# Optimization experiments

Hardware: AMD Instinct MI355X
Metric: run time of the kernel (lower is better)

Reference implementation:

```python
import jax, jax.numpy as jnp
import numpy as np

N_HEAD = 12
D_HEAD = 64
ROT_DIM = 32
THETA = 10000.0
LOOK_B = 1
LOOK_F = 1


def _rope(t):
    # t: [b, h, n, d]; interleaved RoPE on first ROT_DIM dims (lucidrains convention)
    n = t.shape[-2]
    inv_freq = 1.0 / (THETA ** (jnp.arange(0, ROT_DIM, 2, dtype=jnp.float32) / ROT_DIM))
    freqs = jnp.arange(n, dtype=jnp.float32)[:, None] * inv_freq[None, :]   # [n, ROT_DIM//2]
    freqs = jnp.repeat(freqs, 2, axis=-1)                                   # [n, ROT_DIM]
    cos, sin = jnp.cos(freqs), jnp.sin(freqs)
    t_rot, t_pass = t[..., :ROT_DIM], t[..., ROT_DIM:]
    pair = t_rot.reshape(*t_rot.shape[:-1], ROT_DIM // 2, 2)
    rot = jnp.stack([-pair[..., 1], pair[..., 0]], axis=-1).reshape(t_rot.shape)
    return jnp.concatenate([t_rot * cos + rot * sin, t_pass], axis=-1)


def _look_around(x, backward=LOOK_B, forward=LOOK_F, pad_value=-1, dim=2):
    # x: [B, w, n, ...]; pad the window axis, gather shifted windows, concat along dim
    w = x.shape[1]
    pad_width = [(0, 0)] * x.ndim
    pad_width[1] = (backward, forward)
    padded = jnp.pad(x, pad_width, constant_values=pad_value)
    return jnp.concatenate([padded[:, i:i + w] for i in range(forward + backward + 1)], axis=dim)


def _forward(x, w_attn, b_attn, window_size):
    b, n, d_model = x.shape
    qkv = x @ w_attn + b_attn                       # [b, n, 3*d_model]
    q, k, v = jnp.split(qkv, 3, axis=-1)

    def split_heads(t):
        return t.reshape(b, n, N_HEAD, D_HEAD).transpose(0, 2, 1, 3)  # [b, h, n, dh]

    q, k, v = split_heads(q), split_heads(k), split_heads(v)
    q, k = _rope(q), _rope(k)

    scale = D_HEAD ** -0.5
    B = b * N_HEAD
    w = n // window_size
    bq = q.reshape(B, w, window_size, D_HEAD) * scale
    bk = _look_around(k.reshape(B, w, window_size, D_HEAD), pad_value=-1.0)
    bv = _look_around(v.reshape(B, w, window_size, D_HEAD), pad_value=-1.0)

    seq = jnp.arange(n).reshape(1, w, window_size)
    bq_k = _look_around(seq, pad_value=-1)          # [1, w, (lb+lf+1)*ws]
    pad_mask = (bq_k == -1)[:, :, None, :]          # [1, w, 1, j]

    sim = jnp.einsum('bwie,bwje->bwij', bq, bk)     # [B, w, ws, (lb+lf+1)*ws]
    sim = jnp.where(pad_mask, -jnp.finfo(sim.dtype).max, sim)
    attn = jax.nn.softmax(sim, axis=-1)
    out = jnp.einsum('bwij,bwje->bwie', attn, bv)   # [B, w, ws, dh]
    out = out.reshape(b, N_HEAD, n, D_HEAD).transpose(0, 2, 1, 3).reshape(b, n, N_HEAD * D_HEAD)
    return out


def setup_inputs() -> dict:
    key = jax.random.key(0)
    k1, k2, k3 = jax.random.split(key, 3)
    d_model = 768
    x = jax.random.normal(k1, (4, 4096, d_model), dtype=jnp.float32)
    w_attn = jax.random.normal(k2, (d_model, 3 * d_model), dtype=jnp.float32) * 0.02
    b_attn = jax.random.normal(k3, (3 * d_model,), dtype=jnp.float32) * 0.02
    return {"x": x, "w_attn": w_attn, "b_attn": b_attn, "window_size": 128}


def reference(x, w_attn, b_attn, window_size):
    return _forward(x, w_attn, b_attn, window_size)
```

## Files before the change

kernel.cpp:

```cpp
#include <hip/hip_runtime.h>

typedef __attribute__((ext_vector_type(8))) short short8;
typedef __attribute__((ext_vector_type(16))) float f32x16;
typedef __attribute__((ext_vector_type(4))) float f32x4;

__device__ __forceinline__ unsigned short f2bf(float f) {
  unsigned int u = __float_as_uint(f);
  u += 0x7FFFu + ((u >> 16) & 1u);
  return (unsigned short)(u >> 16);
}
__device__ __forceinline__ float bf2f(unsigned short u) {
  return __uint_as_float(((unsigned int)u) << 16);
}

__device__ __forceinline__ void gload16(const unsigned short* g, unsigned short* l) {
  __builtin_amdgcn_global_load_lds(
      (const __attribute__((address_space(1))) void*)g,
      (__attribute__((address_space(3))) void*)l, 16, 0, 0);
}

__global__ __launch_bounds__(256) void cast_x_kernel(const float* __restrict__ x,
                                                     unsigned short* __restrict__ xb,
                                                     int n4) {
  int i = blockIdx.x * 256 + threadIdx.x;
  if (i >= n4) return;
  float4 v = ((const float4*)x)[i];
  ushort4 o;
  o.x = f2bf(v.x); o.y = f2bf(v.y); o.z = f2bf(v.z); o.w = f2bf(v.w);
  ((ushort4*)xb)[i] = o;
}

__global__ void transpose_w_kernel(const float* __restrict__ w,
                                   unsigned short* __restrict__ wt) {
  __shared__ float tile[32][33];
  int n0 = blockIdx.x * 32;
  int k0 = blockIdx.y * 32;
  for (int i = threadIdx.y; i < 32; i += 8)
    tile[i][threadIdx.x] = w[(size_t)(k0 + i) * 2304 + n0 + threadIdx.x];
  __syncthreads();
  for (int i = threadIdx.y; i < 32; i += 8)
    wt[(size_t)(n0 + i) * 768 + k0 + threadIdx.x] = f2bf(tile[threadIdx.x][i]);
}

__global__ __launch_bounds__(256) void qkv_gemm_kernel(
    const unsigned short* __restrict__ xb,
    const unsigned short* __restrict__ wt,
    const float* __restrict__ bias,
    unsigned short* __restrict__ Qb,
    unsigned short* __restrict__ Kb,
    unsigned short* __restrict__ Vb) {
  __shared__ unsigned short lA[128 * 64];
  __shared__ unsigned short lB[128 * 64];
  int bid = blockIdx.x;
  int swz = (bid & 7) * 288 + (bid >> 3);
  int mt = swz / 18, nt = swz - mt * 18;
  int m0 = mt * 128, n0 = nt * 128;

  int tid = threadIdx.x;
  int lane = tid & 63, wid = tid >> 6;
  int wr = wid >> 1, wc = wid & 1;
  int lr = lane & 15, lg = lane >> 4;
  int lswz = lr & 7;

  int offA[4], offB[4];
  unsigned short* ldsA[4];
  unsigned short* ldsB[4];
#pragma unroll
  for (int i = 0; i < 4; i++) {
    int gi = (wid * 4 + i) * 64 + lane;
    int r = gi >> 3;
    int gcl = (gi & 7) ^ (r & 7);
    offA[i] = (m0 + r) * 768 + gcl * 8;
    offB[i] = (n0 + r) * 768 + gcl * 8;
    ldsA[i] = &lA[(wid * 4 + i) * 512];
    ldsB[i] = &lB[(wid * 4 + i) * 512];
  }

  f32x4 acc[4][4] = {};
  const int rowA = (wr * 64 + lr) * 64;
  const int rowB = (wc * 64 + lr) * 64;

  for (int k0 = 0; k0 < 768; k0 += 64) {
    __syncthreads();
#pragma unroll
    for (int i = 0; i < 4; i++) gload16(xb + offA[i] + k0, ldsA[i]);
#pragma unroll
    for (int i = 0; i < 4; i++) gload16(wt + offB[i] + k0, ldsB[i]);
    __syncthreads();

    short8 af[4][2], bfr[4][2];
#pragma unroll
    for (int ks = 0; ks < 2; ks++) {
      int c = ((ks * 4 + lg) ^ lswz) * 8;
#pragma unroll
      for (int mi = 0; mi < 4; mi++)
        af[mi][ks] = *(const short8*)(&lA[rowA + mi * 1024 + c]);
#pragma unroll
      for (int ni = 0; ni < 4; ni++)
        bfr[ni][ks] = *(const short8*)(&lB[rowB + ni * 1024 + c]);
    }
#pragma unroll
    for (int ks = 0; ks < 2; ks++)
#pragma unroll
      for (int mi = 0; mi < 4; mi++)
#pragma unroll
        for (int ni = 0; ni < 4; ni++)
          acc[mi][ni] = __builtin_amdgcn_mfma_f32_16x16x32_bf16(af[mi][ks], bfr[ni][ks], acc[mi][ni], 0, 0, 0);
  }

#pragma unroll
  for (int ni = 0; ni < 4; ni++) {
    int n = n0 + wc * 64 + ni * 16 + lr;
    float bv = bias[n];
    int which = n / 768;
    int idx = n - which * 768;
    int h = idx >> 6, d = idx & 63;
    float scl = (which == 0) ? 0.125f : 1.0f;
    bool doRope = (which < 2) && (ni < 2);
    bool isHi = (d & 1);
    const float L2T = 13.287712379549449f;
    float invf = exp2f(-(float)((d >> 1) & 15) * (L2T / 16.0f));
    unsigned short* dst = (which == 0) ? Qb : ((which == 1) ? Kb : Vb);
#pragma unroll
    for (int mi = 0; mi < 4; mi++) {
#pragma unroll
      for (int reg = 0; reg < 4; reg++) {
        int m = m0 + wr * 64 + mi * 16 + lg * 4 + reg;
        int b = m >> 12, t = m & 4095;
        float val = acc[mi][ni][reg] + bv;
        if (doRope) {
          float other = __shfl_xor(val, 1, 64);
          float ang = (float)t * invf;
          float s, c;
          __sincosf(ang, &s, &c);
          val = isHi ? (val * c + other * s) : (val * c - other * s);
        }
        dst[(((size_t)(b * 12 + h)) * 4096 + t) * 64 + d] = f2bf(val * scl);
      }
    }
  }
}

#define KV_S 72
__global__ __launch_bounds__(256) void attn_kernel(
    const unsigned short* __restrict__ Qb,
    const unsigned short* __restrict__ Kb,
    const unsigned short* __restrict__ Vb,
    float* __restrict__ out) {
  __shared__ unsigned short kS[64 * KV_S];
  __shared__ unsigned short vS[64 * KV_S];
  int wi = blockIdx.x;
  int bh = blockIdx.y;
  int b = bh / 12, h = bh - b * 12;
  int tid = threadIdx.x, lane = tid & 63, wid = tid >> 6;
  int l31 = lane & 31, hi = lane >> 5;

  int qb0 = wi * 128 + wid * 32;
  const unsigned short* Qrow = Qb + ((size_t)bh * 4096 + qb0) * 64;
  short8 qf[4];
#pragma unroll
  for (int kk = 0; kk < 4; kk++)
    qf[kk] = *(const short8*)(Qrow + (size_t)l31 * 64 + kk * 16 + hi * 8);

  f32x16 oacc[2];
#pragma unroll
  for (int dt = 0; dt < 2; dt++)
#pragma unroll
    for (int r = 0; r < 16; r++) oacc[dt][r] = 0.0f;
  float mrow = -1e30f, lsum = 0.0f;

  const unsigned short* Kbase = Kb + (size_t)bh * 4096 * 64;
  const unsigned short* Vbase = Vb + (size_t)bh * 4096 * 64;

  int vk = tid & 63;
  int vq = tid >> 6;

  for (int c = 0; c < 6; c++) {
    int kp0 = (wi - 1) * 128 + c * 64;
    if (kp0 < 0 || kp0 >= 4096) continue;

    __syncthreads();
#pragma unroll
    for (int ci = tid; ci < 512; ci += 256) {
      int kk = ci >> 3, co = (ci & 7) * 8;
      *(uint4*)(&kS[kk * KV_S + co]) = *(const uint4*)(Kbase + (size_t)(kp0 + kk) * 64 + co);
    }
    {
      const unsigned short* vp = Vbase + (size_t)(kp0 + vk) * 64 + vq * 16;
      uint4 v0 = *(const uint4*)(vp);
      uint4 v1 = *(const uint4*)(vp + 8);
      const unsigned short* e = (const unsigned short*)&v0;
#pragma unroll
      for (int i = 0; i < 8; i++) vS[(vq * 16 + i) * KV_S + vk] = e[i];
      e = (const unsigned short*)&v1;
#pragma unroll
      for (int i = 0; i < 8; i++) vS[(vq * 16 + 8 + i) * KV_S + vk] = e[i];
    }
    __syncthreads();

    f32x16 s[2];
#pragma unroll
    for (int kt = 0; kt < 2; kt++) {
      f32x16 acc;
#pragma unroll
      for (int r = 0; r < 16; r++) acc[r] = 0.0f;
#pragma unroll
      for (int kk = 0; kk < 4; kk++) {
        short8 kf = *(const short8*)(&kS[(kt * 32 + l31) * KV_S + kk * 16 + hi * 8]);
        acc = __builtin_amdgcn_mfma_f32_32x32x16_bf16(kf, qf[kk], acc, 0, 0, 0);
      }
      s[kt] = acc;
    }

    float vmax = -1e30f;
#pragma unroll
    for (int kt = 0; kt < 2; kt++)
#pragma unroll
      for (int r = 0; r < 16; r++) vmax = fmaxf(vmax, s[kt][r]);
    vmax = fmaxf(vmax, __shfl_xor(vmax, 32, 64));
    float mnew = fmaxf(mrow, vmax);
    float corr = __expf(mrow - mnew);
    mrow = mnew;
    float rs = 0.0f;
#pragma unroll
    for (int kt = 0; kt < 2; kt++)
#pragma unroll
      for (int r = 0; r < 16; r++) {
        float p = __expf(s[kt][r] - mnew);
        s[kt][r] = p;
        rs += p;
      }
    rs += __shfl_xor(rs, 32, 64);
    lsum = lsum * corr + rs;
#pragma unroll
    for (int dt = 0; dt < 2; dt++)
#pragma unroll
      for (int r = 0; r < 16; r++) oacc[dt][r] *= corr;

#pragma unroll
    for (int kt = 0; kt < 2; kt++) {
#pragma unroll
      for (int kk = 0; kk < 2; kk++) {
        unsigned a0, a1, b0, b1;
        asm("v_cvt_pk_bf16_f32 %0, %1, %2" : "=v"(a0) : "v"(s[kt][kk * 8 + 0]), "v"(s[kt][kk * 8 + 1]));
        asm("v_cvt_pk_bf16_f32 %0, %1, %2" : "=v"(a1) : "v"(s[kt][kk * 8 + 2]), "v"(s[kt][kk * 8 + 3]));
        asm("v_cvt_pk_bf16_f32 %0, %1, %2" : "=v"(b0) : "v"(s[kt][kk * 8 + 4]), "v"(s[kt][kk * 8 + 5]));
        asm("v_cvt_pk_bf16_f32 %0, %1, %2" : "=v"(b1) : "v"(s[kt][kk * 8 + 6]), "v"(s[kt][kk * 8 + 7]));
        asm("v_permlane32_swap_b32 %0, %1" : "+v"(a0), "+v"(b0));
        asm("v_permlane32_swap_b32 %0, %1" : "+v"(a1), "+v"(b1));
        union { unsigned u[4]; short8 v; } pb;
        pb.u[0] = a0; pb.u[1] = a1; pb.u[2] = b0; pb.u[3] = b1;
#pragma unroll
        for (int dt = 0; dt < 2; dt++) {
          short8 vf = *(const short8*)(&vS[(dt * 32 + l31) * KV_S + kt * 32 + kk * 16 + hi * 8]);
          oacc[dt] = __builtin_amdgcn_mfma_f32_32x32x16_bf16(vf, pb.v, oacc[dt], 0, 0, 0);
        }
      }
    }
  }

  float inv = 1.0f / lsum;
  float* orow = out + ((size_t)b * 4096 + qb0 + l31) * 768 + h * 64;
#pragma unroll
  for (int dt = 0; dt < 2; dt++)
#pragma unroll
    for (int g = 0; g < 4; g++) {
      float4 o;
      o.x = oacc[dt][g * 4 + 0] * inv;
      o.y = oacc[dt][g * 4 + 1] * inv;
      o.z = oacc[dt][g * 4 + 2] * inv;
      o.w = oacc[dt][g * 4 + 3] * inv;
      *(float4*)(orow + dt * 32 + g * 8 + hi * 4) = o;
    }
}

extern "C" void kernel_launch(void* const* d_in, const int* in_sizes, int n_in,
                              void* d_out, int out_size, void* d_ws, size_t ws_size,
                              hipStream_t stream) {
  const float* x = (const float*)d_in[0];
  const float* w = (const float*)d_in[1];
  const float* bias = (const float*)d_in[2];
  float* out = (float*)d_out;

  char* ws = (char*)d_ws;
  unsigned short* xb = (unsigned short*)ws;
  unsigned short* wt = (unsigned short*)(ws + 25165824);
  unsigned short* Qb = (unsigned short*)(ws + 28704768);
  unsigned short* Kb = Qb + 12582912;
  unsigned short* Vb = Kb + 12582912;

  hipLaunchKernelGGL(cast_x_kernel, dim3(12288), dim3(256), 0, stream, x, xb, 3145728);
  hipLaunchKernelGGL(transpose_w_kernel, dim3(72, 24), dim3(32, 8), 0, stream, w, wt);
  hipLaunchKernelGGL(qkv_gemm_kernel, dim3(2304), dim3(256), 0, stream, xb, wt, bias, Qb, Kb, Vb);
  hipLaunchKernelGGL(attn_kernel, dim3(32, 48), dim3(256), 0, stream, Qb, Kb, Vb, out);
}
```

Baseline: 144.6 us.

## Restructure QKV GEMM into 256x256 tiles with triple-buffered async LDS pipeline

The QKV projection GEMM now uses 256x256 output tiles with 512 threads (8 waves, each computing 128x64), and a K-step of 32. A three-stage LDS ring buffer is filled by global_load_lds prefetches two steps ahead, using vmcnt waits and raw barriers in place of full __syncthreads. Loads for the next stage are interleaved between the two halves of the MFMA work, and s_setprio is raised around the MFMA blocks. This aims to hide global-memory latency and cut barrier stalls and redundant operand loads. In exchange it uses more registers per thread (32 accumulator fragments) and launches fewer blocks, which can limit occupancy.

```diff
diff --git a/kernel.cpp b/kernel.cpp
--- a/kernel.cpp
+++ b/kernel.cpp
@@ -17,6 +17,12 @@
   __builtin_amdgcn_global_load_lds(
       (const __attribute__((address_space(1))) void*)g,
       (__attribute__((address_space(3))) void*)l, 16, 0, 0);
+}
+
+__device__ __forceinline__ void barrier_raw() {
+  asm volatile("" ::: "memory");
+  __builtin_amdgcn_s_barrier();
+  asm volatile("" ::: "memory");
 }
 
 __global__ __launch_bounds__(256) void cast_x_kernel(const float* __restrict__ x,
@@ -42,100 +48,125 @@
     wt[(size_t)(n0 + i) * 768 + k0 + threadIdx.x] = f2bf(tile[threadIdx.x][i]);
 }
 
-__global__ __launch_bounds__(256) void qkv_gemm_kernel(
+__global__ __launch_bounds__(512, 2) void qkv_gemm_kernel(
     const unsigned short* __restrict__ xb,
     const unsigned short* __restrict__ wt,
     const float* __restrict__ bias,
     unsigned short* __restrict__ Qb,
     unsigned short* __restrict__ Kb,
     unsigned short* __restrict__ Vb) {
-  __shared__ unsigned short lA[128 * 64];
-  __shared__ unsigned short lB[128 * 64];
+  __shared__ unsigned short sA[3][256 * 32];
+  __shared__ unsigned short sB[3][256 * 32];
   int bid = blockIdx.x;
-  int swz = (bid & 7) * 288 + (bid >> 3);
-  int mt = swz / 18, nt = swz - mt * 18;
-  int m0 = mt * 128, n0 = nt * 128;
-
-  int tid = threadIdx.x;
-  int lane = tid & 63, wid = tid >> 6;
-  int wr = wid >> 1, wc = wid & 1;
+  int swz = (bid & 7) * 72 + (bid >> 3);
+  int mt = swz / 9, nt = swz - mt * 9;
+  int m0 = mt * 256, n0 = nt * 256;
+
+  int tid = threadIdx.x, lane = tid & 63, wid = tid >> 6;
+  int wr = wid >> 2, wcn = wid & 3;
   int lr = lane & 15, lg = lane >> 4;
-  int lswz = lr & 7;
-
-  int offA[4], offB[4];
-  unsigned short* ldsA[4];
-  unsigned short* ldsB[4];
-#pragma unroll
-  for (int i = 0; i < 4; i++) {
-    int gi = (wid * 4 + i) * 64 + lane;
-    int r = gi >> 3;
-    int gcl = (gi & 7) ^ (r & 7);
-    offA[i] = (m0 + r) * 768 + gcl * 8;
-    offB[i] = (n0 + r) * 768 + gcl * 8;
-    ldsA[i] = &lA[(wid * 4 + i) * 512];
-    ldsB[i] = &lB[(wid * 4 + i) * 512];
+
+  int srcA[2], srcB[2], dstO[2];
+#pragma unroll
+  for (int j = 0; j < 2; j++) {
+    int idx = j * 512 + tid;
+    int r = idx >> 2, s = idx & 3;
+    int g = s ^ (r & 3);
+    srcA[j] = (m0 + r) * 768 + g * 8;
+    srcB[j] = (n0 + r) * 768 + g * 8;
+    dstO[j] = (j * 512 + wid * 64) * 8;
   }
 
-  f32x4 acc[4][4] = {};
-  const int rowA = (wr * 64 + lr) * 64;
-  const int rowB = (wc * 64 + lr) * 64;
-
-  for (int k0 = 0; k0 < 768; k0 += 64) {
-    __syncthreads();
-#pragma unroll
-    for (int i = 0; i < 4; i++) gload16(xb + offA[i] + k0, ldsA[i]);
-#pragma unroll
-    for (int i = 0; i < 4; i++) gload16(wt + offB[i] + k0, ldsB[i]);
-    __syncthreads();
-
-    short8 af[4][2], bfr[4][2];
-#pragma unroll
-    for (int ks = 0; ks < 2; ks++) {
-      int c = ((ks * 4 + lg) ^ lswz) * 8;
-#pragma unroll
-      for (int mi = 0; mi < 4; mi++)
-        af[mi][ks] = *(const short8*)(&lA[rowA + mi * 1024 + c]);
-#pragma unroll
-      for (int ni = 0; ni < 4; ni++)
-        bfr[ni][ks] = *(const short8*)(&lB[rowB + ni * 1024 + c]);
-    }
-#pragma unroll
-    for (int ks = 0; ks < 2; ks++)
-#pragma unroll
-      for (int mi = 0; mi < 4; mi++)
-#pragma unroll
-        for (int ni = 0; ni < 4; ni++)
-          acc[mi][ni] = __builtin_amdgcn_mfma_f32_16x16x32_bf16(af[mi][ks], bfr[ni][ks], acc[mi][ni], 0, 0, 0);
+  const int cg = (lg ^ (lr & 3)) * 8;
+  const int rdAoff = (wr * 128 + lr) * 32 + cg;
+  const int rdBoff = (wcn * 64 + lr) * 32 + cg;
+
+  f32x4 acc[8][4] = {};
+
+  auto group = [&](int t, const unsigned short* rdA, const unsigned short* rdB,
+                   unsigned short* stA, unsigned short* stB, bool stage, bool last) {
+    if (last) { asm volatile("s_waitcnt vmcnt(0)" ::: "memory"); }
+    else      { asm volatile("s_waitcnt vmcnt(4)" ::: "memory"); }
+    barrier_raw();
+    int k0s = (t + 2) * 32;
+    if (stage) {
+      gload16(xb + srcA[0] + k0s, stA + dstO[0]);
+      gload16(xb + srcA[1] + k0s, stA + dstO[1]);
+    }
+    short8 af[8], bf[4];
+#pragma unroll
+    for (int mf = 0; mf < 8; mf++)
+      af[mf] = *(const short8*)(rdA + rdAoff + mf * 512);
+#pragma unroll
+    for (int nf = 0; nf < 2; nf++)
+      bf[nf] = *(const short8*)(rdB + rdBoff + nf * 512);
+    __builtin_amdgcn_s_setprio(1);
+#pragma unroll
+    for (int mf = 0; mf < 8; mf++)
+#pragma unroll
+      for (int nf = 0; nf < 2; nf++)
+        acc[mf][nf] = __builtin_amdgcn_mfma_f32_16x16x32_bf16(af[mf], bf[nf], acc[mf][nf], 0, 0, 0);
+    __builtin_amdgcn_s_setprio(0);
+    barrier_raw();
+    if (stage) {
+      gload16(wt + srcB[0] + k0s, stB + dstO[0]);
+      gload16(wt + srcB[1] + k0s, stB + dstO[1]);
+    }
+#pragma unroll
+    for (int nf = 2; nf < 4; nf++)
+      bf[nf] = *(const short8*)(rdB + rdBoff + nf * 512);
+    __builtin_amdgcn_s_setprio(1);
+#pragma unroll
+    for (int mf = 0; mf < 8; mf++)
+#pragma unroll
+      for (int nf = 2; nf < 4; nf++)
+        acc[mf][nf] = __builtin_amdgcn_mfma_f32_16x16x32_bf16(af[mf], bf[nf], acc[mf][nf], 0, 0, 0);
+    __builtin_amdgcn_s_setprio(0);
+  };
+
+  gload16(xb + srcA[0], sA[0] + dstO[0]);
+  gload16(xb + srcA[1], sA[0] + dstO[1]);
+  gload16(wt + srcB[0], sB[0] + dstO[0]);
+  gload16(wt + srcB[1], sB[0] + dstO[1]);
+  gload16(xb + srcA[0] + 32, sA[1] + dstO[0]);
+  gload16(xb + srcA[1] + 32, sA[1] + dstO[1]);
+  gload16(wt + srcB[0] + 32, sB[1] + dstO[0]);
+  gload16(wt + srcB[1] + 32, sB[1] + dstO[1]);
+
+  for (int t = 0; t < 24; t += 3) {
+    group(t,     sA[0], sB[0], sA[2], sB[2], t < 22, false);
+    group(t + 1, sA[1], sB[1], sA[0], sB[0], t + 1 < 22, false);
+    group(t + 2, sA[2], sB[2], sA[1], sB[1], t + 2 < 22, t + 2 == 23);
   }
 
 #pragma unroll
-  for (int ni = 0; ni < 4; ni++) {
-    int n = n0 + wc * 64 + ni * 16 + lr;
+  for (int nf = 0; nf < 4; nf++) {
+    int n = n0 + wcn * 64 + nf * 16 + lr;
     float bv = bias[n];
     int which = n / 768;
     int idx = n - which * 768;
     int h = idx >> 6, d = idx & 63;
     float scl = (which == 0) ? 0.125f : 1.0f;
-    bool doRope = (which < 2) && (ni < 2);
+    bool doRope = (which < 2) && (nf < 2);
     bool isHi = (d & 1);
     const float L2T = 13.287712379549449f;
     float invf = exp2f(-(float)((d >> 1) & 15) * (L2T / 16.0f));
     unsigned short* dst = (which == 0) ? Qb : ((which == 1) ? Kb : Vb);
 #pragma unroll
-    for (int mi = 0; mi < 4; mi++) {
+    for (int mf = 0; mf < 8; mf++) {
 #pragma unroll
       for (int reg = 0; reg < 4; reg++) {
-        int m = m0 + wr * 64 + mi * 16 + lg * 4 + reg;
-        int b = m >> 12, t = m & 4095;
-        float val = acc[mi][ni][reg] + bv;
+        int m = m0 + wr * 128 + mf * 16 + lg * 4 + reg;
+        int b = m >> 12, tt = m & 4095;
+        float val = acc[mf][nf][reg] + bv;
         if (doRope) {
           float other = __shfl_xor(val, 1, 64);
-          float ang = (float)t * invf;
+          float ang = (float)tt * invf;
           float s, c;
           __sincosf(ang, &s, &c);
           val = isHi ? (val * c + other * s) : (val * c - other * s);
         }
-        dst[(((size_t)(b * 12 + h)) * 4096 + t) * 64 + d] = f2bf(val * scl);
+        dst[(((size_t)(b * 12 + h)) * 4096 + tt) * 64 + d] = f2bf(val * scl);
       }
     }
   }
@@ -291,6 +322,6 @@
 
   hipLaunchKernelGGL(cast_x_kernel, dim3(12288), dim3(256), 0, stream, x, xb, 3145728);
   hipLaunchKernelGGL(transpose_w_kernel, dim3(72, 24), dim3(32, 8), 0, stream, w, wt);
-  hipLaunchKernelGGL(qkv_gemm_kernel, dim3(2304), dim3(256), 0, stream, xb, wt, bias, Qb, Kb, Vb);
+  hipLaunchKernelGGL(qkv_gemm_kernel, dim3(576), dim3(512), 0, stream, xb, wt, bias, Qb, Kb, Vb);
   hipLaunchKernelGGL(attn_kernel, dim3(32, 48), dim3(256), 0, stream, Qb, Kb, Vb, out);
 }
```

After: 172.5 us. +19.3%, slower.

## Move RoPE and query scaling into attention kernel; merge prep kernels

Applied to the files above, without the earlier changes.

The RoPE rotation and the 1/sqrt(d) query scale move out of the QKV GEMM epilogue and into the attention kernel. Q is rotated once in registers after it is loaded, K is rotated while staged into LDS, and the scale is applied to the scores. The x cast and weight transpose kernels are merged into one launch to save a launch. In exchange K is rotated again for every window that reads it (about 3x redundant sincos work), and rotating after the bf16 store adds an extra rounding step.

```diff
diff --git a/kernel.cpp b/kernel.cpp
--- a/kernel.cpp
+++ b/kernel.cpp
@@ -3,6 +3,8 @@
 typedef __attribute__((ext_vector_type(8))) short short8;
 typedef __attribute__((ext_vector_type(16))) float f32x16;
 typedef __attribute__((ext_vector_type(4))) float f32x4;
+
+#define L2T 13.287712379549449f
 
 __device__ __forceinline__ unsigned short f2bf(float f) {
   unsigned int u = __float_as_uint(f);
@@ -19,27 +21,28 @@
       (__attribute__((address_space(3))) void*)l, 16, 0, 0);
 }
 
-__global__ __launch_bounds__(256) void cast_x_kernel(const float* __restrict__ x,
-                                                     unsigned short* __restrict__ xb,
-                                                     int n4) {
-  int i = blockIdx.x * 256 + threadIdx.x;
-  if (i >= n4) return;
-  float4 v = ((const float4*)x)[i];
-  ushort4 o;
-  o.x = f2bf(v.x); o.y = f2bf(v.y); o.z = f2bf(v.z); o.w = f2bf(v.w);
-  ((ushort4*)xb)[i] = o;
-}
-
-__global__ void transpose_w_kernel(const float* __restrict__ w,
-                                   unsigned short* __restrict__ wt) {
+__global__ __launch_bounds__(256) void prep_kernel(const float* __restrict__ x,
+                                                   unsigned short* __restrict__ xb,
+                                                   const float* __restrict__ w,
+                                                   unsigned short* __restrict__ wt) {
   __shared__ float tile[32][33];
-  int n0 = blockIdx.x * 32;
-  int k0 = blockIdx.y * 32;
-  for (int i = threadIdx.y; i < 32; i += 8)
-    tile[i][threadIdx.x] = w[(size_t)(k0 + i) * 2304 + n0 + threadIdx.x];
-  __syncthreads();
-  for (int i = threadIdx.y; i < 32; i += 8)
-    wt[(size_t)(n0 + i) * 768 + k0 + threadIdx.x] = f2bf(tile[threadIdx.x][i]);
+  int bid = blockIdx.x;
+  if (bid < 12288) {
+    int i = bid * 256 + threadIdx.x;
+    float4 v = ((const float4*)x)[i];
+    ushort4 o;
+    o.x = f2bf(v.x); o.y = f2bf(v.y); o.z = f2bf(v.z); o.w = f2bf(v.w);
+    ((ushort4*)xb)[i] = o;
+  } else {
+    int b2 = bid - 12288;
+    int n0 = (b2 % 72) * 32, k0 = (b2 / 72) * 32;
+    int tx = threadIdx.x & 31, ty = threadIdx.x >> 5;
+    for (int i = ty; i < 32; i += 8)
+      tile[i][tx] = w[(size_t)(k0 + i) * 2304 + n0 + tx];
+    __syncthreads();
+    for (int i = ty; i < 32; i += 8)
+      wt[(size_t)(n0 + i) * 768 + k0 + tx] = f2bf(tile[tx][i]);
+  }
 }
 
 __global__ __launch_bounds__(256) void qkv_gemm_kernel(
@@ -115,11 +118,6 @@
     int which = n / 768;
     int idx = n - which * 768;
     int h = idx >> 6, d = idx & 63;
-    float scl = (which == 0) ? 0.125f : 1.0f;
-    bool doRope = (which < 2) && (ni < 2);
-    bool isHi = (d & 1);
-    const float L2T = 13.287712379549449f;
-    float invf = exp2f(-(float)((d >> 1) & 15) * (L2T / 16.0f));
     unsigned short* dst = (which == 0) ? Qb : ((which == 1) ? Kb : Vb);
 #pragma unroll
     for (int mi = 0; mi < 4; mi++) {
@@ -127,15 +125,7 @@
       for (int reg = 0; reg < 4; reg++) {
         int m = m0 + wr * 64 + mi * 16 + lg * 4 + reg;
         int b = m >> 12, t = m & 4095;
-        float val = acc[mi][ni][reg] + bv;
-        if (doRope) {
-          float other = __shfl_xor(val, 1, 64);
-          float ang = (float)t * invf;
-          float s, c;
-          __sincosf(ang, &s, &c);
-          val = isHi ? (val * c + other * s) : (val * c - other * s);
-        }
-        dst[(((size_t)(b * 12 + h)) * 4096 + t) * 64 + d] = f2bf(val * scl);
+        dst[(((size_t)(b * 12 + h)) * 4096 + t) * 64 + d] = f2bf(acc[mi][ni][reg] + bv);
       }
     }
   }
@@ -162,6 +152,25 @@
   for (int kk = 0; kk < 4; kk++)
     qf[kk] = *(const short8*)(Qrow + (size_t)l31 * 64 + kk * 16 + hi * 8);
 
+  {
+    int t = qb0 + l31;
+#pragma unroll
+    for (int kk = 0; kk < 2; kk++) {
+      unsigned short* e = (unsigned short*)&qf[kk];
+      int j0 = kk * 8 + hi * 4;
+#pragma unroll
+      for (int p = 0; p < 4; p++) {
+        float invf = exp2f(-(float)(j0 + p) * (L2T / 16.0f));
+        float ang = (float)t * invf;
+        float s, c;
+        __sincosf(ang, &s, &c);
+        float a = bf2f(e[2 * p]), b2 = bf2f(e[2 * p + 1]);
+        e[2 * p] = f2bf(a * c - b2 * s);
+        e[2 * p + 1] = f2bf(b2 * c + a * s);
+      }
+    }
+  }
+
   f32x16 oacc[2];
 #pragma unroll
   for (int dt = 0; dt < 2; dt++)
@@ -183,7 +192,23 @@
 #pragma unroll
     for (int ci = tid; ci < 512; ci += 256) {
       int kk = ci >> 3, co = (ci & 7) * 8;
-      *(uint4*)(&kS[kk * KV_S + co]) = *(const uint4*)(Kbase + (size_t)(kp0 + kk) * 64 + co);
+      uint4 val = *(const uint4*)(Kbase + (size_t)(kp0 + kk) * 64 + co);
+      if (co < 32) {
+        unsigned short* e = (unsigned short*)&val;
+        int t = kp0 + kk;
+        int j0 = co >> 1;
+#pragma unroll
+        for (int p = 0; p < 4; p++) {
+          float invf = exp2f(-(float)(j0 + p) * (L2T / 16.0f));
+          float ang = (float)t * invf;
+          float s, cc;
+          __sincosf(ang, &s, &cc);
+          float a = bf2f(e[2 * p]), b2 = bf2f(e[2 * p + 1]);
+          e[2 * p] = f2bf(a * cc - b2 * s);
+          e[2 * p + 1] = f2bf(b2 * cc + a * s);
+        }
+      }
+      *(uint4*)(&kS[kk * KV_S + co]) = val;
     }
     {
       const unsigned short* vp = Vbase + (size_t)(kp0 + vk) * 64 + vq * 16;
@@ -211,6 +236,10 @@
       }
       s[kt] = acc;
     }
+#pragma unroll
+    for (int kt = 0; kt < 2; kt++)
+#pragma unroll
+      for (int r = 0; r < 16; r++) s[kt][r] *= 0.125f;
 
     float vmax = -1e30f;
 #pragma unroll
@@ -289,8 +318,7 @@
   unsigned short* Kb = Qb + 12582912;
   unsigned short* Vb = Kb + 12582912;
 
-  hipLaunchKernelGGL(cast_x_kernel, dim3(12288), dim3(256), 0, stream, x, xb, 3145728);
-  hipLaunchKernelGGL(transpose_w_kernel, dim3(72, 24), dim3(32, 8), 0, stream, w, wt);
+  hipLaunchKernelGGL(prep_kernel, dim3(14016), dim3(256), 0, stream, x, xb, w, wt);
   hipLaunchKernelGGL(qkv_gemm_kernel, dim3(2304), dim3(256), 0, stream, xb, wt, bias, Qb, Kb, Vb);
   hipLaunchKernelGGL(attn_kernel, dim3(32, 48), dim3(256), 0, stream, Qb, Kb, Vb, out);
 }
```

Result: slower. 152.2 us (+5.3%).
